# Optimization experiments

Measured on AMD Instinct MI355X. Metric: run time of the kernel, lower is better.

The kernel has to match this reference:

```python
import jax, jax.numpy as jnp
import numpy as np

SOFTMAX_TEMP = 0.01  # config['networks']['matcher_block']['softmax_temp']
B, WINDOW, C, N, WIDTH = 2, 2, 64, 400, 256


def setup_inputs() -> dict:
    key = jax.random.key(0)
    k1, k2, k3 = jax.random.split(key, 3)
    BW = B * WINDOW
    keypoint_scores = jax.random.uniform(k1, (BW, 1, N), dtype=jnp.float32)
    keypoint_desc = jax.random.normal(k2, (BW, C, N), dtype=jnp.float32)
    desc_dense = jax.random.normal(k3, (BW, C, WIDTH, WIDTH), dtype=jnp.float32)
    # pairing indices exactly as built in SoftmaxRefMatcher.__init__
    tgt_ids, src_ids = [], []
    for b in range(B):
        for w in range(WINDOW - 1):
            for t in range(w + 1, WINDOW):
                src_ids.append(w + b * WINDOW)
                tgt_ids.append(t + b * WINDOW)
    return {
        "keypoint_scores": keypoint_scores,
        "keypoint_desc": keypoint_desc,
        "desc_dense": desc_dense,
        "tgt_ids": jnp.array(tgt_ids, dtype=jnp.int32),
        "src_ids": jnp.array(src_ids, dtype=jnp.int32),
    }


def _l2_normalize(x):
    # F.normalize(x, dim=1), eps=1e-12
    return x / jnp.maximum(jnp.linalg.norm(x, axis=1, keepdims=True), 1e-12)


def reference(keypoint_scores, keypoint_desc, desc_dense, tgt_ids, src_ids):
    BW, Cdim, H, W = desc_dense.shape
    HW = H * W
    # src_coords_dense: meshgrid('ij') -> coords[k] = (u=k%W, v=k//W)
    hw = jnp.arange(HW)
    coords = jnp.stack([(hw % W).astype(jnp.float32),
                        (hw // W).astype(jnp.float32)], axis=1)  # [HW, 2]

    src_desc = _l2_normalize(desc_dense.reshape(BW, Cdim, HW))[src_ids]  # [P, C, HW]
    tgt_desc = _l2_normalize(keypoint_desc)[tgt_ids]                     # [P, C, N]

    match_vals = jnp.einsum('pcn,pcm->pnm', tgt_desc, src_desc)          # [P, N, HW]
    soft_match = jax.nn.softmax(match_vals / SOFTMAX_TEMP, axis=2)
    pseudo_coords = jnp.einsum('pnm,mk->pnk', soft_match, coords)        # [P, N, 2]

    tgt_scores = keypoint_scores[tgt_ids]
    return pseudo_coords, tgt_scores, tgt_ids, src_ids
```

## Files before the change

### kernel.cpp

```cpp
#include <hip/hip_runtime.h>
#include <math.h>

#define NPAIR  2
#define KDIM   64
#define NKP    400
#define NPADR  448
#define DSTR   14
#define HWPIX  65536
#define MREF   70.0f

#define AFRAG_DW (NPAIR*DSTR*2*2*2*256)

using frag_ab = __attribute__((ext_vector_type(8))) short;
using f32x4   = __attribute__((ext_vector_type(4))) float;

__device__ __forceinline__ unsigned short f2bf(float f){
    unsigned u = __builtin_bit_cast(unsigned, f);
    u += 0x7fffu + ((u >> 16) & 1u);
    return (unsigned short)(u >> 16);
}
__device__ __forceinline__ float bf2f(unsigned short h){
    unsigned u = ((unsigned)h) << 16;
    return __builtin_bit_cast(float, u);
}
__device__ __forceinline__ float red16(float v){
    v += __builtin_bit_cast(float, __builtin_amdgcn_update_dpp(0, __builtin_bit_cast(int, v), 0xB1,  0xF, 0xF, true));
    v += __builtin_bit_cast(float, __builtin_amdgcn_update_dpp(0, __builtin_bit_cast(int, v), 0x4E,  0xF, 0xF, true));
    v += __builtin_bit_cast(float, __builtin_amdgcn_update_dpp(0, __builtin_bit_cast(int, v), 0x141, 0xF, 0xF, true));
    v += __builtin_bit_cast(float, __builtin_amdgcn_update_dpp(0, __builtin_bit_cast(int, v), 0x140, 0xF, 0xF, true));
    return v;
}

__global__ __launch_bounds__(256) void prep_kernel(
    const float* __restrict__ ksc, const float* __restrict__ kd,
    const int* __restrict__ tgt_ids, const int* __restrict__ src_ids,
    unsigned* __restrict__ wsu, float* __restrict__ out)
{
    __shared__ float xs[KDIM][33];
    __shared__ float inv_s[32];
    int d = blockIdx.x, p = blockIdx.y, t = threadIdx.x;
    int tgt = tgt_ids[p];
    int nl = t & 31, c0 = t >> 5;
    #pragma unroll
    for (int cc = 0; cc < 8; ++cc){
        int c = cc*8 + c0;
        int n = d*32 + nl;
        xs[c][nl] = (n < NKP) ? kd[(tgt*KDIM + c)*NKP + n] : 0.f;
    }
    __syncthreads();
    if (t < 32){
        float s = 0.f;
        #pragma unroll
        for (int c = 0; c < KDIM; ++c){ float v = xs[c][t]; s = fmaf(v, v, s); }
        inv_s[t] = 1.f / fmaxf(sqrtf(s), 1e-12f);
    }
    __syncthreads();
    {
        int l = t & 63, rk = t >> 6;
        int rt = rk >> 1, ks = rk & 1;
        int cl = l & 15, g = l >> 4;
        int nloc = rt*16 + cl;
        float inv = inv_s[nloc];
        int k0 = ks*32 + g*8;
        unsigned hu[4], lu[4];
        #pragma unroll
        for (int j2 = 0; j2 < 4; ++j2){
            float xa = xs[k0 + 2*j2    ][nloc] * inv;
            float xb = xs[k0 + 2*j2 + 1][nloc] * inv;
            unsigned short ha = f2bf(xa), hb = f2bf(xb);
            unsigned short la = f2bf(xa - bf2f(ha)), lb = f2bf(xb - bf2f(hb));
            hu[j2] = (unsigned)ha | ((unsigned)hb << 16);
            lu[j2] = (unsigned)la | ((unsigned)lb << 16);
        }
        unsigned base = (unsigned)((((p*DSTR + d)*2 + rt)*2 + ks)*2)*256 + l*4;
        *(uint4*)&wsu[base]       = make_uint4(hu[0], hu[1], hu[2], hu[3]);
        *(uint4*)&wsu[base + 256] = make_uint4(lu[0], lu[1], lu[2], lu[3]);
    }
    if (t < 32){
        int n = d*32 + t;
        if (n < NKP) out[NPAIR*NKP*2 + p*NKP + n] = ksc[tgt*NKP + n];
    }
    if (d == 0 && t == 0){
        out[NPAIR*NKP*3 + p]         = (float)tgt;
        out[NPAIR*NKP*3 + NPAIR + p] = (float)src_ids[p];
    }
}

__global__ __launch_bounds__(256, 2) void match_kernel(
    const float* __restrict__ dd, const int* __restrict__ src_ids,
    const unsigned* __restrict__ wsu, float* __restrict__ part)
{
    __shared__ unsigned lds[16384];
    __shared__ float invn_s[256];
    int mb = blockIdx.x, p = blockIdx.y, t = threadIdx.x;
    const float* plane = dd + (size_t)src_ids[p]*KDIM*HWPIX + mb*256;

    {
        int m = t;
        unsigned sw7 = (unsigned)(m & 7) << 2;
        float ssum = 0.f;
        #pragma unroll
        for (int s2 = 0; s2 < 8; ++s2){
            float v[8];
            #pragma unroll
            for (int j = 0; j < 8; ++j) v[j] = plane[(size_t)(s2*8 + j)*HWPIX + m];
            unsigned hq[4], lq[4];
            #pragma unroll
            for (int q = 0; q < 4; ++q){
                float a = v[2*q], b = v[2*q + 1];
                ssum = fmaf(a, a, ssum);
                ssum = fmaf(b, b, ssum);
                unsigned short ha = f2bf(a), hb = f2bf(b);
                unsigned short la = f2bf(a - bf2f(ha)), lb = f2bf(b - bf2f(hb));
                hq[q] = (unsigned)ha | ((unsigned)hb << 16);
                lq[q] = (unsigned)la | ((unsigned)lb << 16);
            }
            unsigned dwb = (unsigned)m*32 + (((unsigned)s2 << 2) ^ sw7);
            *(uint4*)&lds[dwb]        = make_uint4(hq[0], hq[1], hq[2], hq[3]);
            *(uint4*)&lds[8192 + dwb] = make_uint4(lq[0], lq[1], lq[2], lq[3]);
        }
        invn_s[m] = 100.f / fmaxf(sqrtf(ssum), 1e-12f);
    }
    __syncthreads();

    int w = t >> 6, l = t & 63;
    int cl = l & 15, g = l >> 4;
    int mhalf = w & 1;
    int mtb = mhalf << 3;
    float invm[8];
    #pragma unroll
    for (int mi = 0; mi < 8; ++mi) invm[mi] = invn_s[(mtb + mi)*16 + cl];

    #pragma unroll 1
    for (int d = (w >> 1); d < DSTR; d += 2){
        f32x4 acc[2][8];
        #pragma unroll
        for (int rt = 0; rt < 2; ++rt)
            #pragma unroll
            for (int mi = 0; mi < 8; ++mi)
                acc[rt][mi] = (f32x4){0.f, 0.f, 0.f, 0.f};

        #pragma unroll
        for (int ks = 0; ks < 2; ++ks){
            unsigned base0 = (unsigned)((((p*DSTR + d)*2 + 0)*2 + ks)*2)*256 + l*4;
            unsigned base1 = (unsigned)((((p*DSTR + d)*2 + 1)*2 + ks)*2)*256 + l*4;
            frag_ab aH0 = __builtin_bit_cast(frag_ab, *(const uint4*)&wsu[base0]);
            frag_ab aL0 = __builtin_bit_cast(frag_ab, *(const uint4*)&wsu[base0 + 256]);
            frag_ab aH1 = __builtin_bit_cast(frag_ab, *(const uint4*)&wsu[base1]);
            frag_ab aL1 = __builtin_bit_cast(frag_ab, *(const uint4*)&wsu[base1 + 256]);
            #pragma unroll
            for (int mi = 0; mi < 8; ++mi){
                int mrow = (mtb + mi)*16 + cl;
                unsigned swm = (unsigned)(mrow & 7) << 2;
                unsigned dwb = (unsigned)mrow*32 + (((unsigned)(ks*4 + g) << 2) ^ swm);
                frag_ab BH = __builtin_bit_cast(frag_ab, *(const uint4*)&lds[dwb]);
                frag_ab BL = __builtin_bit_cast(frag_ab, *(const uint4*)&lds[8192 + dwb]);
                acc[0][mi] = __builtin_amdgcn_mfma_f32_16x16x32_bf16(aH0, BH, acc[0][mi], 0, 0, 0);
                acc[1][mi] = __builtin_amdgcn_mfma_f32_16x16x32_bf16(aH1, BH, acc[1][mi], 0, 0, 0);
                acc[0][mi] = __builtin_amdgcn_mfma_f32_16x16x32_bf16(aH0, BL, acc[0][mi], 0, 0, 0);
                acc[1][mi] = __builtin_amdgcn_mfma_f32_16x16x32_bf16(aH1, BL, acc[1][mi], 0, 0, 0);
                acc[0][mi] = __builtin_amdgcn_mfma_f32_16x16x32_bf16(aL0, BH, acc[0][mi], 0, 0, 0);
                acc[1][mi] = __builtin_amdgcn_mfma_f32_16x16x32_bf16(aL1, BH, acc[1][mi], 0, 0, 0);
            }
        }
        #pragma unroll
        for (int rt = 0; rt < 2; ++rt)
        #pragma unroll
        for (int r = 0; r < 4; ++r){
            float sE = 0.f, sU = 0.f;
            #pragma unroll
            for (int mi = 0; mi < 8; ++mi){
                float e = __expf(fmaf(acc[rt][mi][r], invm[mi], -MREF));
                sE += e;
                sU = fmaf(e, (float)((mtb + mi)*16), sU);
            }
            sU = fmaf((float)cl, sE, sU);
            sE = red16(sE); sU = red16(sU);
            if (cl == 0){
                int n = d*32 + rt*16 + g*4 + r;
                *(float2*)&part[(((size_t)(p*NPADR + n)*256 + mb)*2 + mhalf)*2] =
                    make_float2(sE, sU);
            }
        }
    }
}

__global__ __launch_bounds__(256) void merge_kernel(
    const float* __restrict__ part, float* __restrict__ out)
{
    int wid = blockIdx.x*4 + (threadIdx.x >> 6);
    int l = threadIdx.x & 63;
    int p = wid / NKP, n = wid - p*NKP;
    const float* base = part + (size_t)(p*NPADR + n)*1024;
    float S = 0.f, U = 0.f, V = 0.f;
    #pragma unroll
    for (int k4 = 0; k4 < 4; ++k4){
        int mbk = l + 64*k4;
        float4 q = *(const float4*)&base[mbk*4];
        float s = q.x + q.z;
        S += s;
        U += q.y + q.w;
        V = fmaf((float)mbk, s, V);
    }
    #pragma unroll
    for (int off = 1; off < 64; off <<= 1){
        S += __shfl_xor(S, off);
        U += __shfl_xor(U, off);
        V += __shfl_xor(V, off);
    }
    if (l == 0){
        out[(p*NKP + n)*2 + 0] = U / S;
        out[(p*NKP + n)*2 + 1] = V / S;
    }
}

extern "C" void kernel_launch(void* const* d_in, const int* in_sizes, int n_in,
                              void* d_out, int out_size, void* d_ws, size_t ws_size,
                              hipStream_t stream)
{
    const float* ksc     = (const float*)d_in[0];
    const float* kd      = (const float*)d_in[1];
    const float* dd      = (const float*)d_in[2];
    const int*   tgt_ids = (const int*)d_in[3];
    const int*   src_ids = (const int*)d_in[4];
    float* out = (float*)d_out;
    unsigned* wsu = (unsigned*)d_ws;
    float* part = (float*)d_ws + AFRAG_DW;

    prep_kernel <<<dim3(DSTR, NPAIR), 256, 0, stream>>>(ksc, kd, tgt_ids, src_ids, wsu, out);
    match_kernel<<<dim3(256,  NPAIR), 256, 0, stream>>>(dd, src_ids, wsu, part);
    merge_kernel<<<200,               256, 0, stream>>>(part, out);
}
```

Measured before the change: 131.0 us.

## Halve pixel tile per block to double grid and raise occupancy

The match kernel now handles 128 pixels per block instead of 256, so the grid doubles to 512 blocks per pair and LDS per block is halved. Launch bounds move to 4 blocks per SM. The two thread halves split the channel loading and combine their partial sums of squares through shared memory with an extra barrier. Exp is switched to exp2 with log2e folded into the scale, and the merge kernel reads twice as many partials with adjusted coordinate offsets. The intent is more occupancy and better latency hiding for the memory-bound load of the dense descriptors, at the cost of more partial writes and a larger merge.

```diff
diff --git a/kernel.cpp b/kernel.cpp
--- a/kernel.cpp
+++ b/kernel.cpp
@@ -8,6 +8,7 @@
 #define DSTR   14
 #define HWPIX  65536
 #define MREF   70.0f
+#define LOG2E  1.44269504f
 
 #define AFRAG_DW (NPAIR*DSTR*2*2*2*256)
 
@@ -86,21 +87,23 @@
     }
 }
 
-__global__ __launch_bounds__(256, 2) void match_kernel(
+__global__ __launch_bounds__(256, 4) void match_kernel(
     const float* __restrict__ dd, const int* __restrict__ src_ids,
     const unsigned* __restrict__ wsu, float* __restrict__ part)
 {
-    __shared__ unsigned lds[16384];
-    __shared__ float invn_s[256];
+    __shared__ unsigned lds[8192];
+    __shared__ float ssp[256];
+    __shared__ float invn_s[128];
     int mb = blockIdx.x, p = blockIdx.y, t = threadIdx.x;
-    const float* plane = dd + (size_t)src_ids[p]*KDIM*HWPIX + mb*256;
+    const float* plane = dd + (size_t)src_ids[p]*KDIM*HWPIX + mb*128;
 
     {
-        int m = t;
+        int m = t & 127, kh = t >> 7;
         unsigned sw7 = (unsigned)(m & 7) << 2;
         float ssum = 0.f;
         #pragma unroll
-        for (int s2 = 0; s2 < 8; ++s2){
+        for (int s2l = 0; s2l < 4; ++s2l){
+            int s2 = kh*4 + s2l;
             float v[8];
             #pragma unroll
             for (int j = 0; j < 8; ++j) v[j] = plane[(size_t)(s2*8 + j)*HWPIX + m];
@@ -117,44 +120,55 @@
             }
             unsigned dwb = (unsigned)m*32 + (((unsigned)s2 << 2) ^ sw7);
             *(uint4*)&lds[dwb]        = make_uint4(hq[0], hq[1], hq[2], hq[3]);
-            *(uint4*)&lds[8192 + dwb] = make_uint4(lq[0], lq[1], lq[2], lq[3]);
-        }
-        invn_s[m] = 100.f / fmaxf(sqrtf(ssum), 1e-12f);
-    }
+            *(uint4*)&lds[4096 + dwb] = make_uint4(lq[0], lq[1], lq[2], lq[3]);
+        }
+        ssp[t] = ssum;
+    }
+    __syncthreads();
+    if (t < 128)
+        invn_s[t] = (100.f * LOG2E) / fmaxf(sqrtf(ssp[t] + ssp[t + 128]), 1e-12f);
     __syncthreads();
 
     int w = t >> 6, l = t & 63;
     int cl = l & 15, g = l >> 4;
-    int mhalf = w & 1;
-    int mtb = mhalf << 3;
-    float invm[8];
-    #pragma unroll
-    for (int mi = 0; mi < 8; ++mi) invm[mi] = invn_s[(mtb + mi)*16 + cl];
+    int mq = w & 1;
+    int mtb = mq << 2;
+    const float mref2 = MREF * LOG2E;
+    float invm[4];
+    #pragma unroll
+    for (int mi = 0; mi < 4; ++mi) invm[mi] = invn_s[(mtb + mi)*16 + cl];
 
     #pragma unroll 1
     for (int d = (w >> 1); d < DSTR; d += 2){
-        f32x4 acc[2][8];
+        uint4 AH[2][2], AL[2][2];
         #pragma unroll
         for (int rt = 0; rt < 2; ++rt)
-            #pragma unroll
-            for (int mi = 0; mi < 8; ++mi)
+        #pragma unroll
+        for (int ks = 0; ks < 2; ++ks){
+            unsigned base = (unsigned)((((p*DSTR + d)*2 + rt)*2 + ks)*2)*256 + l*4;
+            AH[rt][ks] = *(const uint4*)&wsu[base];
+            AL[rt][ks] = *(const uint4*)&wsu[base + 256];
+        }
+        f32x4 acc[2][4];
+        #pragma unroll
+        for (int rt = 0; rt < 2; ++rt)
+            #pragma unroll
+            for (int mi = 0; mi < 4; ++mi)
                 acc[rt][mi] = (f32x4){0.f, 0.f, 0.f, 0.f};
 
         #pragma unroll
         for (int ks = 0; ks < 2; ++ks){
-            unsigned base0 = (unsigned)((((p*DSTR + d)*2 + 0)*2 + ks)*2)*256 + l*4;
-            unsigned base1 = (unsigned)((((p*DSTR + d)*2 + 1)*2 + ks)*2)*256 + l*4;
-            frag_ab aH0 = __builtin_bit_cast(frag_ab, *(const uint4*)&wsu[base0]);
-            frag_ab aL0 = __builtin_bit_cast(frag_ab, *(const uint4*)&wsu[base0 + 256]);
-            frag_ab aH1 = __builtin_bit_cast(frag_ab, *(const uint4*)&wsu[base1]);
-            frag_ab aL1 = __builtin_bit_cast(frag_ab, *(const uint4*)&wsu[base1 + 256]);
-            #pragma unroll
-            for (int mi = 0; mi < 8; ++mi){
+            frag_ab aH0 = __builtin_bit_cast(frag_ab, AH[0][ks]);
+            frag_ab aL0 = __builtin_bit_cast(frag_ab, AL[0][ks]);
+            frag_ab aH1 = __builtin_bit_cast(frag_ab, AH[1][ks]);
+            frag_ab aL1 = __builtin_bit_cast(frag_ab, AL[1][ks]);
+            #pragma unroll
+            for (int mi = 0; mi < 4; ++mi){
                 int mrow = (mtb + mi)*16 + cl;
                 unsigned swm = (unsigned)(mrow & 7) << 2;
                 unsigned dwb = (unsigned)mrow*32 + (((unsigned)(ks*4 + g) << 2) ^ swm);
                 frag_ab BH = __builtin_bit_cast(frag_ab, *(const uint4*)&lds[dwb]);
-                frag_ab BL = __builtin_bit_cast(frag_ab, *(const uint4*)&lds[8192 + dwb]);
+                frag_ab BL = __builtin_bit_cast(frag_ab, *(const uint4*)&lds[4096 + dwb]);
                 acc[0][mi] = __builtin_amdgcn_mfma_f32_16x16x32_bf16(aH0, BH, acc[0][mi], 0, 0, 0);
                 acc[1][mi] = __builtin_amdgcn_mfma_f32_16x16x32_bf16(aH1, BH, acc[1][mi], 0, 0, 0);
                 acc[0][mi] = __builtin_amdgcn_mfma_f32_16x16x32_bf16(aH0, BL, acc[0][mi], 0, 0, 0);
@@ -169,16 +183,16 @@
         for (int r = 0; r < 4; ++r){
             float sE = 0.f, sU = 0.f;
             #pragma unroll
-            for (int mi = 0; mi < 8; ++mi){
-                float e = __expf(fmaf(acc[rt][mi][r], invm[mi], -MREF));
+            for (int mi = 0; mi < 4; ++mi){
+                float e = exp2f(fmaf(acc[rt][mi][r], invm[mi], -mref2));
                 sE += e;
-                sU = fmaf(e, (float)((mtb + mi)*16), sU);
+                sU = fmaf(e, (float)(mi*16), sU);
             }
             sU = fmaf((float)cl, sE, sU);
             sE = red16(sE); sU = red16(sU);
             if (cl == 0){
                 int n = d*32 + rt*16 + g*4 + r;
-                *(float2*)&part[(((size_t)(p*NPADR + n)*256 + mb)*2 + mhalf)*2] =
+                *(float2*)&part[(((size_t)(p*NPADR + n)*512 + mb)*2 + mq)*2] =
                     make_float2(sE, sU);
             }
         }
@@ -191,16 +205,17 @@
     int wid = blockIdx.x*4 + (threadIdx.x >> 6);
     int l = threadIdx.x & 63;
     int p = wid / NKP, n = wid - p*NKP;
-    const float* base = part + (size_t)(p*NPADR + n)*1024;
+    const float* base = part + (size_t)(p*NPADR + n)*2048;
     float S = 0.f, U = 0.f, V = 0.f;
     #pragma unroll
-    for (int k4 = 0; k4 < 4; ++k4){
-        int mbk = l + 64*k4;
+    for (int k = 0; k < 8; ++k){
+        int mbk = l + 64*k;
         float4 q = *(const float4*)&base[mbk*4];
+        float u0 = (float)((mbk & 1)*128);
         float s = q.x + q.z;
         S += s;
-        U += q.y + q.w;
-        V = fmaf((float)mbk, s, V);
+        U += q.y + q.w + u0*q.x + (u0 + 64.f)*q.z;
+        V = fmaf((float)(mbk >> 1), s, V);
     }
     #pragma unroll
     for (int off = 1; off < 64; off <<= 1){
@@ -228,6 +243,6 @@
     float* part = (float*)d_ws + AFRAG_DW;
 
     prep_kernel <<<dim3(DSTR, NPAIR), 256, 0, stream>>>(ksc, kd, tgt_ids, src_ids, wsu, out);
-    match_kernel<<<dim3(256,  NPAIR), 256, 0, stream>>>(dd, src_ids, wsu, part);
+    match_kernel<<<dim3(512,  NPAIR), 256, 0, stream>>>(dd, src_ids, wsu, part);
     merge_kernel<<<200,               256, 0, stream>>>(part, out);
 }
```

Measured after the change: 138.3 us. 5.6% more time.
